# Kernel tuning notes

Hardware: AMD Instinct MI355X
Metric: run time of the kernel (lower is better)

Reference implementation:

```python
import jax, jax.numpy as jnp
import numpy as np

WINDOW = (4, 8, 8)   # (Wd, Wh, Ww), N = 256
DIM = 128
HEADS = 4
B_ = 512             # num_windows * batch
NW = 64              # windows per volume -> batch B = B_ // NW = 8
TABLE = (2 * WINDOW[0] - 1) * (2 * WINDOW[1] - 1) * (2 * WINDOW[2] - 1)  # 1575


def _relative_position_index():
    d, h, w = WINDOW
    coords = np.stack(np.meshgrid(np.arange(d), np.arange(h), np.arange(w), indexing='ij'))
    cf = coords.reshape(3, -1)                      # (3, N)
    rel = cf[:, :, None] - cf[:, None, :]           # (3, N, N)
    rel = rel.transpose(1, 2, 0).copy()             # (N, N, 3)
    rel[..., 0] += d - 1
    rel[..., 1] += h - 1
    rel[..., 2] += w - 1
    rel[..., 0] *= (2 * h - 1) * (2 * w - 1)
    rel[..., 1] *= 2 * w - 1
    return rel.sum(-1)                              # (N, N) int


def setup_inputs() -> dict:
    key = jax.random.key(0)
    k1, k2, k3, k4, k5, k6 = jax.random.split(key, 6)
    N = WINDOW[0] * WINDOW[1] * WINDOW[2]
    x = jax.random.normal(k1, (B_, N, DIM), dtype=jnp.float32)
    mask = jnp.zeros((NW, N, N), dtype=jnp.float32)
    qkv_weight = jax.random.normal(k2, (3 * DIM, DIM), dtype=jnp.float32) * 0.05
    q_bias = jax.random.normal(k3, (DIM,), dtype=jnp.float32) * 0.02
    v_bias = jax.random.normal(k4, (DIM,), dtype=jnp.float32) * 0.02
    rel_bias_table = jax.random.normal(k5, (TABLE, HEADS), dtype=jnp.float32) * 0.02
    return {"x": x, "mask": mask, "qkv_weight": qkv_weight,
            "q_bias": q_bias, "v_bias": v_bias, "rel_bias_table": rel_bias_table}


def reference(x, mask, qkv_weight, q_bias, v_bias, rel_bias_table):
    B, N, C = x.shape
    H = HEADS
    hd = C // H
    # qkv projection with bias = [q_bias, 0, v_bias]
    qkv_bias = jnp.concatenate([q_bias, jnp.zeros_like(v_bias), v_bias])
    qkv = x @ qkv_weight.T + qkv_bias                      # (B_, N, 3C)
    qkv = qkv.reshape(B, N, 3, H, hd).transpose(2, 0, 3, 1, 4)
    q, k, v = qkv[0], qkv[1], qkv[2]                       # (B_, H, N, hd)
    # relative position bias gathered from the table
    idx = jnp.asarray(_relative_position_index().reshape(-1))
    bias = rel_bias_table[idx].reshape(N, N, H).transpose(2, 0, 1)[None]  # (1, H, N, N)
    # shift mask: (nW, N, N) -> (B_, 1, N, N), batch-major tiling like torch repeat
    nW = mask.shape[0]
    reps = B // nW
    attn_mask = jnp.tile(mask[:, None], (reps, 1, 1, 1)) + bias           # (B_, H, N, N)
    scale = 1.0 / jnp.sqrt(jnp.asarray(hd, dtype=x.dtype))
    logits = jnp.einsum('bhnd,bhmd->bhnm', q, k) * scale + attn_mask
    attn = jax.nn.softmax(logits, axis=-1)
    out = jnp.einsum('bhnm,bhmd->bhnd', attn, v)           # (B_, H, N, hd)
    return out.transpose(0, 2, 1, 3).reshape(B, N, C)
```

## Files before the change

### kernel.cpp

```cpp
#include <hip/hip_runtime.h>

#define NTOK 256
#define DIM  128
#define HD   32
#define NWIN 64

typedef __bf16 bf16x8 __attribute__((ext_vector_type(8)));
typedef __bf16 bf16x4 __attribute__((ext_vector_type(4)));
typedef float  f32x4  __attribute__((ext_vector_type(4)));

__device__ __forceinline__ float bf2f(unsigned short s) {
    union { unsigned u; float f; } x; x.u = ((unsigned)s) << 16; return x.f;
}

#define X_OFF 0
#define W_OFF 65536
#define Q_OFF 90112
#define K_OFF 106496
#define V_OFF 122880
#define LDS_BYTES 139264

__device__ __forceinline__ int swz256(int row, int b) { return row * 256 + (b ^ ((row & 7) << 4)); }
__device__ __forceinline__ int swz64 (int row, int b) { return row * 64  + (b ^ (((row >> 1) & 3) << 4)); }
__device__ __forceinline__ int swzV  (int d,   int b) { return d   * 512 + (b ^ ((d & 7) << 4)); }

__device__ __forceinline__ unsigned f2bf_rne(float f) {
    union { float f; unsigned u; } x; x.f = f;
    return (x.u + 0x7FFF + ((x.u >> 16) & 1)) >> 16;
}

__device__ __forceinline__ int rel_idx(int i, int j) {
    int di = i >> 6, hi = (i >> 3) & 7, wi = i & 7;
    int dj = j >> 6, hj = (j >> 3) & 7, wj = j & 7;
    return 225 * (di - dj + 3) + 15 * (hi - hj + 7) + (wi - wj + 7);
}

__global__ void comb_kernel(const float* __restrict__ mask, const float* __restrict__ table,
                            unsigned short* __restrict__ comb) {
    int gid = blockIdx.x * 256 + threadIdx.x;
    int j = gid & 255, i = (gid >> 8) & 255, h = (gid >> 16) & 3, w = gid >> 18;
    float v = mask[(w << 16) | (i << 8) | j] + table[rel_idx(i, j) * 4 + h];
    comb[gid] = (unsigned short)f2bf_rne(v);
}

__global__ void bias_kernel(const float* __restrict__ table, unsigned short* __restrict__ bias) {
    int gid = blockIdx.x * 256 + threadIdx.x;
    int j = gid & 255, i = (gid >> 8) & 255, h = gid >> 16;
    bias[gid] = (unsigned short)f2bf_rne(table[rel_idx(i, j) * 4 + h]);
}

template <int MODE>
__global__ __launch_bounds__(512, 2) void attn_kernel(
    const float* __restrict__ x, const float* __restrict__ qkv_w,
    const float* __restrict__ q_bias, const float* __restrict__ v_bias,
    const unsigned short* __restrict__ aux16, const float* __restrict__ mask,
    const float* __restrict__ table, float* __restrict__ out) {
    extern __shared__ char smem[];
    const int tid = threadIdx.x;
    const int bb = blockIdx.x >> 2, h = blockIdx.x & 3;
    const int w = tid >> 6, lane = tid & 63, lr = lane & 15, lg = lane >> 4;

    const float* xp = x + (size_t)bb * (NTOK * DIM);
    #pragma unroll
    for (int it = 0; it < 8; ++it) {
        int base = (it * 512 + tid) * 8;
        int row = base >> 7, col = base & 127;
        float4 f0 = *(const float4*)(xp + base);
        float4 f1 = *(const float4*)(xp + base + 4);
        union { bf16x8 v; __bf16 e[8]; } u8;
        u8.e[0] = (__bf16)f0.x; u8.e[1] = (__bf16)f0.y; u8.e[2] = (__bf16)f0.z; u8.e[3] = (__bf16)f0.w;
        u8.e[4] = (__bf16)f1.x; u8.e[5] = (__bf16)f1.y; u8.e[6] = (__bf16)f1.z; u8.e[7] = (__bf16)f1.w;
        *(bf16x8*)(smem + X_OFF + swz256(row, col * 2)) = u8.v;
    }
    #pragma unroll
    for (int it = 0; it < 3; ++it) {
        int base = (it * 512 + tid) * 8;
        int row = base >> 7, col = base & 127;
        int sec = row >> 5, r5 = row & 31;
        const float* wp = qkv_w + ((sec * 128 + h * 32 + r5) * DIM + col);
        float4 f0 = *(const float4*)(wp);
        float4 f1 = *(const float4*)(wp + 4);
        union { bf16x8 v; __bf16 e[8]; } u8;
        u8.e[0] = (__bf16)f0.x; u8.e[1] = (__bf16)f0.y; u8.e[2] = (__bf16)f0.z; u8.e[3] = (__bf16)f0.w;
        u8.e[4] = (__bf16)f1.x; u8.e[5] = (__bf16)f1.y; u8.e[6] = (__bf16)f1.z; u8.e[7] = (__bf16)f1.w;
        *(bf16x8*)(smem + W_OFF + swz256(row, col * 2)) = u8.v;
    }
    __syncthreads();

    const float SCALE = 0.17677669529663687f;
    #pragma unroll
    for (int mi = 0; mi < 2; ++mi) {
        int mt = w * 2 + mi;
        bf16x8 xa[4];
        #pragma unroll
        for (int kk = 0; kk < 4; ++kk)
            xa[kk] = *(bf16x8*)(smem + X_OFF + swz256(mt * 16 + lr, kk * 64 + lg * 16));
        #pragma unroll
        for (int nt = 0; nt < 6; ++nt) {
            f32x4 acc = {0.f, 0.f, 0.f, 0.f};
            #pragma unroll
            for (int kk = 0; kk < 4; ++kk) {
                bf16x8 wb = *(bf16x8*)(smem + W_OFF + swz256(nt * 16 + lr, kk * 64 + lg * 16));
                acc = __builtin_amdgcn_mfma_f32_16x16x32_bf16(xa[kk], wb, acc, 0, 0, 0);
            }
            int sec = nt >> 1;
            int d = (nt & 1) * 16 + lr;
            float bias = 0.f;
            if (sec == 0) bias = q_bias[h * 32 + d];
            if (sec == 2) bias = v_bias[h * 32 + d];
            #pragma unroll
            for (int r = 0; r < 4; ++r) {
                int row = mt * 16 + lg * 4 + r;
                float val = acc[r] + bias;
                if (sec == 0) {
                    val *= SCALE;
                    *(__bf16*)(smem + Q_OFF + swz64(row, d * 2)) = (__bf16)val;
                } else if (sec == 1) {
                    *(__bf16*)(smem + K_OFF + swz64(row, d * 2)) = (__bf16)val;
                } else {
                    *(__bf16*)(smem + V_OFF + swzV(d, row * 2)) = (__bf16)val;
                }
            }
        }
    }
    __syncthreads();

    bf16x8 qf[2];
    #pragma unroll
    for (int tt = 0; tt < 2; ++tt)
        qf[tt] = *(bf16x8*)(smem + Q_OFF + swz64(w * 32 + tt * 16 + lr, lg * 16));

    f32x4 st[2][16];
    #pragma unroll
    for (int kt = 0; kt < 16; ++kt) {
        bf16x8 kf = *(bf16x8*)(smem + K_OFF + swz64(kt * 16 + lr, lg * 16));
        f32x4 z = {0.f, 0.f, 0.f, 0.f};
        st[0][kt] = __builtin_amdgcn_mfma_f32_16x16x32_bf16(kf, qf[0], z, 0, 0, 0);
        st[1][kt] = __builtin_amdgcn_mfma_f32_16x16x32_bf16(kf, qf[1], z, 0, 0, 0);
    }

    const int w_idx = bb & 63;
    float inv[2];
    #pragma unroll
    for (int tt = 0; tt < 2; ++tt) {
        int rg = w * 32 + tt * 16 + lr;
        float mx = -3.0e38f;
        #pragma unroll
        for (int kt = 0; kt < 16; ++kt) {
            if (MODE == 0) {
                const unsigned short* crow =
                    aux16 + (((size_t)(w_idx * 4 + h)) << 16) + rg * 256 + lg * 4;
                ushort4 c4 = *(const ushort4*)(crow + kt * 16);
                st[tt][kt][0] += bf2f(c4.x);
                st[tt][kt][1] += bf2f(c4.y);
                st[tt][kt][2] += bf2f(c4.z);
                st[tt][kt][3] += bf2f(c4.w);
            } else if (MODE == 1) {
                const unsigned short* brow = aux16 + (((size_t)h) << 16) + rg * 256 + lg * 4;
                const float* mrow = mask + (((size_t)w_idx) << 16) + rg * 256 + lg * 4;
                ushort4 c4 = *(const ushort4*)(brow + kt * 16);
                float4 m4 = *(const float4*)(mrow + kt * 16);
                st[tt][kt][0] += bf2f(c4.x) + m4.x;
                st[tt][kt][1] += bf2f(c4.y) + m4.y;
                st[tt][kt][2] += bf2f(c4.z) + m4.z;
                st[tt][kt][3] += bf2f(c4.w) + m4.w;
            } else {
                const float* mrow = mask + (((size_t)w_idx) << 16) + rg * 256 + lg * 4;
                float4 m4 = *(const float4*)(mrow + kt * 16);
                #pragma unroll
                for (int c = 0; c < 4; ++c) {
                    int j = kt * 16 + lg * 4 + c;
                    float m = (c == 0) ? m4.x : (c == 1) ? m4.y : (c == 2) ? m4.z : m4.w;
                    st[tt][kt][c] += table[rel_idx(rg, j) * 4 + h] + m;
                }
            }
            mx = fmaxf(mx, fmaxf(fmaxf(st[tt][kt][0], st[tt][kt][1]),
                                 fmaxf(st[tt][kt][2], st[tt][kt][3])));
        }
        mx = fmaxf(mx, __shfl_xor(mx, 16));
        mx = fmaxf(mx, __shfl_xor(mx, 32));
        float sum = 0.f;
        #pragma unroll
        for (int kt = 0; kt < 16; ++kt) {
            #pragma unroll
            for (int c = 0; c < 4; ++c) {
                float e = __expf(st[tt][kt][c] - mx);
                st[tt][kt][c] = e;
                sum += e;
            }
        }
        sum += __shfl_xor(sum, 16);
        sum += __shfl_xor(sum, 32);
        inv[tt] = 1.0f / sum;
    }

    char* pbuf = smem + X_OFF + w * 2048;
    f32x4 oacc[2][2];
    #pragma unroll
    for (int tt = 0; tt < 2; ++tt)
        #pragma unroll
        for (int u = 0; u < 2; ++u)
            oacc[tt][u] = (f32x4){0.f, 0.f, 0.f, 0.f};

    #pragma unroll
    for (int s = 0; s < 8; ++s) {
        #pragma unroll
        for (int tt = 0; tt < 2; ++tt) {
            #pragma unroll
            for (int half = 0; half < 2; ++half) {
                f32x4 p = st[tt][2 * s + half];
                union { bf16x4 v; __bf16 e[4]; } u4;
                u4.e[0] = (__bf16)(p[0] * inv[tt]);
                u4.e[1] = (__bf16)(p[1] * inv[tt]);
                u4.e[2] = (__bf16)(p[2] * inv[tt]);
                u4.e[3] = (__bf16)(p[3] * inv[tt]);
                *(bf16x4*)(pbuf + swz64(tt * 16 + lr, half * 32 + lg * 8)) = u4.v;
            }
        }
        bf16x8 vf[2];
        #pragma unroll
        for (int u = 0; u < 2; ++u)
            vf[u] = *(bf16x8*)(smem + V_OFF + swzV(u * 16 + lr, s * 64 + lg * 16));
        #pragma unroll
        for (int tt = 0; tt < 2; ++tt) {
            bf16x8 af = *(bf16x8*)(pbuf + swz64(tt * 16 + lr, lg * 16));
            #pragma unroll
            for (int u = 0; u < 2; ++u)
                oacc[tt][u] = __builtin_amdgcn_mfma_f32_16x16x32_bf16(af, vf[u], oacc[tt][u], 0, 0, 0);
        }
    }

    float* op = out + (((size_t)bb * 256 + w * 32) * 128) + h * 32;
    #pragma unroll
    for (int tt = 0; tt < 2; ++tt)
        #pragma unroll
        for (int u = 0; u < 2; ++u)
            #pragma unroll
            for (int r = 0; r < 4; ++r)
                op[(tt * 16 + lg * 4 + r) * 128 + u * 16 + lr] = oacc[tt][u][r];
}

extern "C" void kernel_launch(void* const* d_in, const int* in_sizes, int n_in,
                              void* d_out, int out_size, void* d_ws, size_t ws_size,
                              hipStream_t stream) {
    const float* x      = (const float*)d_in[0];
    const float* mask   = (const float*)d_in[1];
    const float* qkv_w  = (const float*)d_in[2];
    const float* q_bias = (const float*)d_in[3];
    const float* v_bias = (const float*)d_in[4];
    const float* table  = (const float*)d_in[5];
    float* out = (float*)d_out;
    (void)in_sizes; (void)n_in; (void)out_size;

    const size_t NEED_COMB = (size_t)NWIN * 4 * 256 * 256 * 2;
    const size_t NEED_BIAS = (size_t)4 * 256 * 256 * 2;

    if (ws_size >= NEED_COMB) {
        unsigned short* comb = (unsigned short*)d_ws;
        comb_kernel<<<65536, 256, 0, stream>>>(mask, table, comb);
        hipFuncSetAttribute((const void*)attn_kernel<0>,
                            hipFuncAttributeMaxDynamicSharedMemorySize, LDS_BYTES);
        attn_kernel<0><<<2048, 512, LDS_BYTES, stream>>>(x, qkv_w, q_bias, v_bias,
                                                         comb, mask, table, out);
    } else if (ws_size >= NEED_BIAS) {
        unsigned short* bias = (unsigned short*)d_ws;
        bias_kernel<<<1024, 256, 0, stream>>>(table, bias);
        hipFuncSetAttribute((const void*)attn_kernel<1>,
                            hipFuncAttributeMaxDynamicSharedMemorySize, LDS_BYTES);
        attn_kernel<1><<<2048, 512, LDS_BYTES, stream>>>(x, qkv_w, q_bias, v_bias,
                                                         bias, mask, table, out);
    } else {
        hipFuncSetAttribute((const void*)attn_kernel<2>,
                            hipFuncAttributeMaxDynamicSharedMemorySize, LDS_BYTES);
        attn_kernel<2><<<2048, 512, LDS_BYTES, stream>>>(x, qkv_w, q_bias, v_bias,
                                                         nullptr, mask, table, out);
    }
}
```

Measured before the change: 175.4 us.

## Split fused attention into prep, projection, and attention kernels

Adds a new path, used when the workspace is large enough, that precomputes bf16 bias, mask and weights, then runs a separate QKV projection kernel writing scaled Q, K and transposed V to global memory. A lighter attention kernel then uses only 48KB of LDS so more blocks fit per CU. The aim is to avoid each of the four per-head blocks recomputing the full x projection and to raise occupancy. The cost is extra global round-trips for Q/K/V (about 100MB of workspace) plus separate bias and mask reads. It also reads bias and mask per element instead of a combined tensor.

```diff
diff --git a/kernel.cpp b/kernel.cpp
--- a/kernel.cpp
+++ b/kernel.cpp
@@ -11,6 +11,215 @@
 
 __device__ __forceinline__ float bf2f(unsigned short s) {
     union { unsigned u; float f; } x; x.u = ((unsigned)s) << 16; return x.f;
+}
+__device__ __forceinline__ unsigned f2bf_rne(float f) {
+    union { float f; unsigned u; } x; x.f = f;
+    return (x.u + 0x7FFF + ((x.u >> 16) & 1)) >> 16;
+}
+__device__ __forceinline__ int rel_idx(int i, int j) {
+    int di = i >> 6, hi = (i >> 3) & 7, wi = i & 7;
+    int dj = j >> 6, hj = (j >> 3) & 7, wj = j & 7;
+    return 225 * (di - dj + 3) + 15 * (hi - hj + 7) + (wi - wj + 7);
+}
+
+__device__ __forceinline__ int swz256(int row, int b) { return row * 256 + (b ^ ((row & 7) << 4)); }
+__device__ __forceinline__ int swz64 (int row, int b) { return row * 64  + (b ^ (((row >> 1) & 3) << 4)); }
+__device__ __forceinline__ int swzV  (int d,   int b) { return d   * 512 + (b ^ ((d & 7) << 4)); }
+
+#define BIAS_OFF 0u
+#define MASK_OFF 0x80000u
+#define WBF_OFF  0x880000u
+#define QR_OFF   0x8A0000u
+#define KR_OFF   0x28A0000u
+#define VT_OFF   0x48A0000u
+#define NEED_SPLIT 0x68A0000u
+
+__global__ void prep_kernel(const float* __restrict__ mask, const float* __restrict__ table,
+                            const float* __restrict__ qkv_w,
+                            unsigned short* __restrict__ bias, unsigned short* __restrict__ maskbf,
+                            unsigned short* __restrict__ wbf) {
+    int gid = blockIdx.x * 256 + threadIdx.x;
+    if (gid < 262144) {
+        int j = gid & 255, i = (gid >> 8) & 255, h = gid >> 16;
+        bias[gid] = (unsigned short)f2bf_rne(table[rel_idx(i, j) * 4 + h]);
+    } else if (gid < 262144 + 4194304) {
+        int m = gid - 262144;
+        maskbf[m] = (unsigned short)f2bf_rne(mask[m]);
+    } else if (gid < 262144 + 4194304 + 49152) {
+        int v = gid - 4456448;
+        wbf[v] = (unsigned short)f2bf_rne(qkv_w[v]);
+    }
+}
+
+__global__ __launch_bounds__(256, 8) void proj_kernel(
+    const float* __restrict__ x, const unsigned short* __restrict__ wbf,
+    const float* __restrict__ q_bias, const float* __restrict__ v_bias,
+    unsigned short* __restrict__ qr, unsigned short* __restrict__ kr,
+    unsigned short* __restrict__ vt) {
+    const int tid = threadIdx.x;
+    const int wv = tid >> 6, lane = tid & 63, lr = lane & 15, lg = lane >> 4;
+    const int n0 = blockIdx.x * 64 + wv * 16;
+    const int bb = n0 >> 8;
+    const int nloc0 = n0 & 255;
+    const float SCALE = 0.17677669529663687f;
+
+    const float* xrow = x + (size_t)(n0 + lr) * DIM;
+    bf16x8 xa[4];
+    #pragma unroll
+    for (int kk = 0; kk < 4; ++kk) {
+        const float* p = xrow + kk * 32 + lg * 8;
+        float4 f0 = *(const float4*)(p);
+        float4 f1 = *(const float4*)(p + 4);
+        union { bf16x8 v; __bf16 e[8]; } u8;
+        u8.e[0] = (__bf16)f0.x; u8.e[1] = (__bf16)f0.y; u8.e[2] = (__bf16)f0.z; u8.e[3] = (__bf16)f0.w;
+        u8.e[4] = (__bf16)f1.x; u8.e[5] = (__bf16)f1.y; u8.e[6] = (__bf16)f1.z; u8.e[7] = (__bf16)f1.w;
+        xa[kk] = u8.v;
+    }
+    #pragma unroll
+    for (int h = 0; h < 4; ++h) {
+        const size_t bh = (size_t)(bb * 4 + h);
+        #pragma unroll
+        for (int nt = 0; nt < 6; ++nt) {
+            const int sec = nt >> 1;
+            const int wrow = sec * 128 + h * 32 + (nt & 1) * 16 + lr;
+            f32x4 acc = {0.f, 0.f, 0.f, 0.f};
+            #pragma unroll
+            for (int kk = 0; kk < 4; ++kk) {
+                bf16x8 wb = *(const bf16x8*)(wbf + wrow * DIM + kk * 32 + lg * 8);
+                acc = __builtin_amdgcn_mfma_f32_16x16x32_bf16(xa[kk], wb, acc, 0, 0, 0);
+            }
+            const int d = (nt & 1) * 16 + lr;
+            if (sec == 2) {
+                float b = v_bias[h * 32 + d];
+                union { bf16x4 v; __bf16 e[4]; } u4;
+                #pragma unroll
+                for (int r = 0; r < 4; ++r) u4.e[r] = (__bf16)(acc[r] + b);
+                int nb = nloc0 + lg * 4;
+                *(bf16x4*)(vt + (bh * 32 + d) * 256 + nb) = u4.v;
+            } else {
+                float b = (sec == 0) ? q_bias[h * 32 + d] : 0.f;
+                unsigned short* dst = (sec == 0) ? qr : kr;
+                #pragma unroll
+                for (int r = 0; r < 4; ++r) {
+                    int n = nloc0 + lg * 4 + r;
+                    float val = acc[r] + b;
+                    if (sec == 0) val *= SCALE;
+                    dst[(bh * 256 + n) * 32 + d] = (unsigned short)f2bf_rne(val);
+                }
+            }
+        }
+    }
+}
+
+#define K_L 0
+#define V_L 16384
+#define P_L 32768
+
+__global__ __launch_bounds__(512, 4) void attn2_kernel(
+    const unsigned short* __restrict__ qr, const unsigned short* __restrict__ kr,
+    const unsigned short* __restrict__ vt, const unsigned short* __restrict__ bias,
+    const unsigned short* __restrict__ maskbf, float* __restrict__ out) {
+    __shared__ char smem[49152];
+    const int tid = threadIdx.x;
+    const int bid = blockIdx.x;
+    const int rep = bid >> 8, pair = bid & 255;
+    const int w_idx = pair >> 2, h = pair & 3;
+    const int bb = rep * 64 + w_idx;
+    const size_t bh = (size_t)(bb * 4 + h);
+
+    {
+        int row = tid >> 1, half = tid & 1;
+        const unsigned short* src = kr + (bh * 256 + row) * 32 + half * 16;
+        bf16x8 a = *(const bf16x8*)(src);
+        bf16x8 b = *(const bf16x8*)(src + 8);
+        *(bf16x8*)(smem + K_L + swz64(row, half * 32)) = a;
+        *(bf16x8*)(smem + K_L + swz64(row, half * 32 + 16)) = b;
+    }
+    {
+        int d = tid >> 4, seg = tid & 15;
+        const unsigned short* src = vt + (bh * 32 + d) * 256 + seg * 16;
+        bf16x8 a = *(const bf16x8*)(src);
+        bf16x8 b = *(const bf16x8*)(src + 8);
+        *(bf16x8*)(smem + V_L + swzV(d, seg * 32)) = a;
+        *(bf16x8*)(smem + V_L + swzV(d, seg * 32 + 16)) = b;
+    }
+    __syncthreads();
+
+    const int w = tid >> 6, lane = tid & 63, lr = lane & 15, lg = lane >> 4;
+    const unsigned short* brow_base = bias + ((size_t)h << 16);
+    const unsigned short* mrow_base = maskbf + ((size_t)w_idx << 16);
+    char* pbuf = smem + P_L + w * 2048;
+
+    #pragma unroll
+    for (int tt = 0; tt < 2; ++tt) {
+        const int rg = w * 32 + tt * 16 + lr;
+        bf16x8 qf = *(const bf16x8*)(qr + (bh * 256 + rg) * 32 + lg * 8);
+
+        f32x4 st[16];
+        #pragma unroll
+        for (int kt = 0; kt < 16; ++kt) {
+            bf16x8 kf = *(bf16x8*)(smem + K_L + swz64(kt * 16 + lr, lg * 16));
+            f32x4 z = {0.f, 0.f, 0.f, 0.f};
+            st[kt] = __builtin_amdgcn_mfma_f32_16x16x32_bf16(kf, qf, z, 0, 0, 0);
+        }
+        const unsigned short* brow = brow_base + rg * 256 + lg * 4;
+        const unsigned short* mrow = mrow_base + rg * 256 + lg * 4;
+        float mx = -3.0e38f;
+        #pragma unroll
+        for (int kt = 0; kt < 16; ++kt) {
+            ushort4 b4 = *(const ushort4*)(brow + kt * 16);
+            ushort4 m4 = *(const ushort4*)(mrow + kt * 16);
+            st[kt][0] += bf2f(b4.x) + bf2f(m4.x);
+            st[kt][1] += bf2f(b4.y) + bf2f(m4.y);
+            st[kt][2] += bf2f(b4.z) + bf2f(m4.z);
+            st[kt][3] += bf2f(b4.w) + bf2f(m4.w);
+            mx = fmaxf(mx, fmaxf(fmaxf(st[kt][0], st[kt][1]), fmaxf(st[kt][2], st[kt][3])));
+        }
+        mx = fmaxf(mx, __shfl_xor(mx, 16));
+        mx = fmaxf(mx, __shfl_xor(mx, 32));
+        float sum = 0.f;
+        #pragma unroll
+        for (int kt = 0; kt < 16; ++kt) {
+            #pragma unroll
+            for (int c = 0; c < 4; ++c) {
+                float e = __expf(st[kt][c] - mx);
+                st[kt][c] = e;
+                sum += e;
+            }
+        }
+        sum += __shfl_xor(sum, 16);
+        sum += __shfl_xor(sum, 32);
+        float inv = 1.0f / sum;
+
+        f32x4 oacc[2];
+        oacc[0] = (f32x4){0.f, 0.f, 0.f, 0.f};
+        oacc[1] = (f32x4){0.f, 0.f, 0.f, 0.f};
+        #pragma unroll
+        for (int s = 0; s < 8; ++s) {
+            #pragma unroll
+            for (int half = 0; half < 2; ++half) {
+                f32x4 p = st[2 * s + half];
+                union { bf16x4 v; __bf16 e[4]; } u4;
+                u4.e[0] = (__bf16)(p[0] * inv);
+                u4.e[1] = (__bf16)(p[1] * inv);
+                u4.e[2] = (__bf16)(p[2] * inv);
+                u4.e[3] = (__bf16)(p[3] * inv);
+                *(bf16x4*)(pbuf + swz64(lr, half * 32 + lg * 8)) = u4.v;
+            }
+            bf16x8 af = *(bf16x8*)(pbuf + swz64(lr, lg * 16));
+            #pragma unroll
+            for (int u = 0; u < 2; ++u) {
+                bf16x8 vf = *(bf16x8*)(smem + V_L + swzV(u * 16 + lr, s * 64 + lg * 16));
+                oacc[u] = __builtin_amdgcn_mfma_f32_16x16x32_bf16(af, vf, oacc[u], 0, 0, 0);
+            }
+        }
+        float* op = out + (((size_t)bb * 256 + w * 32 + tt * 16) * 128) + h * 32;
+        #pragma unroll
+        for (int u = 0; u < 2; ++u)
+            #pragma unroll
+            for (int r = 0; r < 4; ++r)
+                op[(lg * 4 + r) * 128 + u * 16 + lr] = oacc[u][r];
+    }
 }
 
 #define X_OFF 0
@@ -20,21 +229,6 @@
 #define V_OFF 122880
 #define LDS_BYTES 139264
 
-__device__ __forceinline__ int swz256(int row, int b) { return row * 256 + (b ^ ((row & 7) << 4)); }
-__device__ __forceinline__ int swz64 (int row, int b) { return row * 64  + (b ^ (((row >> 1) & 3) << 4)); }
-__device__ __forceinline__ int swzV  (int d,   int b) { return d   * 512 + (b ^ ((d & 7) << 4)); }
-
-__device__ __forceinline__ unsigned f2bf_rne(float f) {
-    union { float f; unsigned u; } x; x.f = f;
-    return (x.u + 0x7FFF + ((x.u >> 16) & 1)) >> 16;
-}
-
-__device__ __forceinline__ int rel_idx(int i, int j) {
-    int di = i >> 6, hi = (i >> 3) & 7, wi = i & 7;
-    int dj = j >> 6, hj = (j >> 3) & 7, wj = j & 7;
-    return 225 * (di - dj + 3) + 15 * (hi - hj + 7) + (wi - wj + 7);
-}
-
 __global__ void comb_kernel(const float* __restrict__ mask, const float* __restrict__ table,
                             unsigned short* __restrict__ comb) {
     int gid = blockIdx.x * 256 + threadIdx.x;
@@ -42,7 +236,6 @@
     float v = mask[(w << 16) | (i << 8) | j] + table[rel_idx(i, j) * 4 + h];
     comb[gid] = (unsigned short)f2bf_rne(v);
 }
-
 __global__ void bias_kernel(const float* __restrict__ table, unsigned short* __restrict__ bias) {
     int gid = blockIdx.x * 256 + threadIdx.x;
     int j = gid & 255, i = (gid >> 8) & 255, h = gid >> 16;
@@ -252,9 +445,22 @@
     float* out = (float*)d_out;
     (void)in_sizes; (void)n_in; (void)out_size;
 
+    if (ws_size >= (size_t)NEED_SPLIT) {
+        char* ws = (char*)d_ws;
+        unsigned short* bias   = (unsigned short*)(ws + BIAS_OFF);
+        unsigned short* maskbf = (unsigned short*)(ws + MASK_OFF);
+        unsigned short* wbf    = (unsigned short*)(ws + WBF_OFF);
+        unsigned short* qr     = (unsigned short*)(ws + QR_OFF);
+        unsigned short* kr     = (unsigned short*)(ws + KR_OFF);
+        unsigned short* vt     = (unsigned short*)(ws + VT_OFF);
+        prep_kernel<<<17600, 256, 0, stream>>>(mask, table, qkv_w, bias, maskbf, wbf);
+        proj_kernel<<<2048, 256, 0, stream>>>(x, wbf, q_bias, v_bias, qr, kr, vt);
+        attn2_kernel<<<2048, 512, 0, stream>>>(qr, kr, vt, bias, maskbf, out);
+        return;
+    }
+
     const size_t NEED_COMB = (size_t)NWIN * 4 * 256 * 256 * 2;
     const size_t NEED_BIAS = (size_t)4 * 256 * 256 * 2;
-
     if (ws_size >= NEED_COMB) {
         unsigned short* comb = (unsigned short*)d_ws;
         comb_kernel<<<65536, 256, 0, stream>>>(mask, table, comb);
```

Result: slower. 248.4 us (+41.6%).
